# Optimization experiments

Measured on AMD Instinct MI355X. Metric: run time of the kernel, lower is better.

Reference implementation:

```python
import jax, jax.numpy as jnp
import numpy as np
import math

D_MODEL = 1024
N_HEAD = 16
Q_DIM = K_DIM = V_DIM = 1024
SCALE = math.sqrt(D_MODEL // N_HEAD)  # 8.0
B, LQ, LK = 2, 2048, 2048


def setup_inputs() -> dict:
    key = jax.random.key(0)
    ks = jax.random.split(key, 10)
    s = 1.0 / math.sqrt(Q_DIM)
    return {
        "q": jax.random.normal(ks[0], (B, LQ, Q_DIM), jnp.float32),
        "k": jax.random.normal(ks[1], (B, LK, K_DIM), jnp.float32),
        "v": jax.random.normal(ks[2], (B, LK, V_DIM), jnp.float32),
        "mask": jax.random.randint(ks[3], (B, LQ, LK), 0, 2, jnp.int32),
        "Wq": jax.random.uniform(ks[4], (D_MODEL, Q_DIM), jnp.float32, -s, s),
        "bq": jnp.zeros((D_MODEL,), jnp.float32),
        "Wk": jax.random.uniform(ks[5], (D_MODEL, K_DIM), jnp.float32, -s, s),
        "bk": jnp.zeros((D_MODEL,), jnp.float32),
        "Wv": jax.random.uniform(ks[6], (D_MODEL, V_DIM), jnp.float32, -s, s),
        "bv": jnp.zeros((D_MODEL,), jnp.float32),
    }


def reference(q, k, v, Wq, bq, Wk, bk, Wv, bv, mask):
    b, lq, _ = q.shape
    lk = k.shape[1]
    dh = D_MODEL // N_HEAD
    # linear projections (torch Linear: x @ W.T + b)
    qh = (q @ Wq.T + bq).reshape(b, lq, N_HEAD, dh).transpose(0, 2, 1, 3)  # bhqd
    kh = (k @ Wk.T + bk).reshape(b, lk, N_HEAD, dh).transpose(0, 2, 1, 3)  # bhkd
    vh = (v @ Wv.T + bv).reshape(b, lk, N_HEAD, dh).transpose(0, 2, 1, 3)  # bhkd
    attn = jnp.einsum("bhqd,bhkd->bhqk", qh, kh) / SCALE
    m = mask[:, None, :, :]  # b1qk
    attn = jnp.where(m == 0, -jnp.inf, attn)
    # rows whose mask is all-zero are reset to 0 pre-softmax (-> uniform weights)
    row_empty = (m.sum(-1, keepdims=True) == 0)
    attn = jnp.where(row_empty, 0.0, attn)
    attn = jax.nn.softmax(attn, axis=-1)  # dropout is identity in eval mode
    v_out = jnp.einsum("bhqk,bhkd->bhqd", attn, vh)
    v_out = v_out.transpose(0, 2, 1, 3).reshape(b, lq, D_MODEL)
    k_out = jnp.einsum("bhqk,bhkd->bhqd", attn, kh)
    k_out = k_out.transpose(0, 2, 1, 3).reshape(b, lq, D_MODEL)
    return (k_out, v_out)
```

## Files before the change

kernel.cpp:

```cpp
#include <hip/hip_runtime.h>
#include <hip/hip_bf16.h>
#include <stdint.h>

typedef __bf16 bf16x8 __attribute__((ext_vector_type(8)));
typedef __bf16 bf16x4 __attribute__((ext_vector_type(4)));
typedef float f32x4 __attribute__((ext_vector_type(4)));

#define B_ 2
#define LQ_ 2048
#define LK_ 2048
#define NH_ 16
#define DH_ 64
#define DM_ 1024

#define AS1 __attribute__((address_space(1)))
#define AS3 __attribute__((address_space(3)))

__device__ __forceinline__ void gload_lds16(const void* g, void* l) {
  __builtin_amdgcn_global_load_lds((const AS1 uint32_t*)g, (AS3 uint32_t*)l, 16, 0, 0);
}

__global__ __launch_bounds__(256) void pack_mask_kernel(
    const int* __restrict__ m, unsigned* __restrict__ out) {
  int gtid = blockIdx.x * 256 + threadIdx.x;
  unsigned long long bal = __ballot(m[gtid] != 0);
  if ((threadIdx.x & 31) == 0)
    out[gtid >> 5] = (unsigned)(bal >> ((threadIdx.x & 32) ? 32 : 0));
}

__global__ __launch_bounds__(256) void cvt_f32_bf16_kernel(
    const float* __restrict__ s, __bf16* __restrict__ d) {
  size_t t = (size_t)blockIdx.x * 256 + threadIdx.x;
  float4 f = ((const float4*)s)[t];
  bf16x4 o;
  o[0] = (__bf16)f.x; o[1] = (__bf16)f.y; o[2] = (__bf16)f.z; o[3] = (__bf16)f.w;
  ((bf16x4*)d)[t] = o;
}

__global__ __launch_bounds__(256) void proj_kernel(
    const __bf16* __restrict__ X0, const __bf16* __restrict__ X1,
    const __bf16* __restrict__ X2,
    const float* __restrict__ b0p, const float* __restrict__ b1p,
    const float* __restrict__ b2p,
    const __bf16* __restrict__ W0, const __bf16* __restrict__ W1,
    const __bf16* __restrict__ W2,
    __bf16* __restrict__ qh, __bf16* __restrict__ kh,
    __bf16* __restrict__ khT, __bf16* __restrict__ vhT, int zbase) {
  __shared__ __align__(16) __bf16 abuf[128 * 32];
  __shared__ __align__(16) __bf16 bbuf[128 * 32];
  __shared__ __align__(16) __bf16 c_lds[128][72];

  const int mode = zbase + blockIdx.z;
  const __bf16* X = mode == 0 ? X0 : (mode == 1 ? X1 : X2);
  const __bf16* W = mode == 0 ? W0 : (mode == 1 ? W1 : W2);
  const float* bias = mode == 0 ? b0p : (mode == 1 ? b1p : b2p);
  __bf16* ostd = mode == 0 ? qh : (mode == 1 ? kh : nullptr);
  __bf16* otr = mode == 0 ? nullptr : (mode == 1 ? khT : vhT);

  const int t = threadIdx.x;
  const int wave = t >> 6, lane = t & 63;
  const int lo16 = lane & 15, quad = lane >> 4;
  const int wm = wave >> 1, wn = wave & 1;
  const int m0 = blockIdx.x * 128, n0 = blockIdx.y * 128;
  const int srow = lane >> 2, scg = (lane & 3) ^ (srow & 3);

  f32x4 acc[4][4] = {};

  for (int k0 = 0; k0 < DM_; k0 += 32) {
    __syncthreads();
#pragma unroll
    for (int ii = 2 * wave; ii < 2 * wave + 2; ii++) {
      int row = ii * 16 + srow;
      gload_lds16(X + (size_t)(m0 + row) * DM_ + k0 + scg * 8, abuf + ii * 512);
      gload_lds16(W + (size_t)(n0 + row) * DM_ + k0 + scg * 8, bbuf + ii * 512);
    }
    __syncthreads();
    bf16x8 af[4], bfr[4];
#pragma unroll
    for (int g = 0; g < 4; g++) {
      int ar = wm * 64 + g * 16 + lo16;
      af[g] = *(const bf16x8*)(abuf + ar * 32 + (quad ^ (ar & 3)) * 8);
      int br = wn * 64 + g * 16 + lo16;
      bfr[g] = *(const bf16x8*)(bbuf + br * 32 + (quad ^ (br & 3)) * 8);
    }
#pragma unroll
    for (int gm = 0; gm < 4; gm++)
#pragma unroll
      for (int gn = 0; gn < 4; gn++)
        acc[gm][gn] =
            __builtin_amdgcn_mfma_f32_16x16x32_bf16(af[gm], bfr[gn], acc[gm][gn], 0, 0, 0);
  }

  const int b = m0 >> 11, l0 = m0 & 2047;
  for (int nhf = 0; nhf < 2; nhf++) {
    __syncthreads();
    if (wn == nhf) {
#pragma unroll
      for (int gn = 0; gn < 4; gn++) {
        float bi = bias[n0 + nhf * 64 + gn * 16 + lo16];
#pragma unroll
        for (int gm = 0; gm < 4; gm++)
#pragma unroll
          for (int r = 0; r < 4; r++)
            c_lds[wm * 64 + gm * 16 + quad * 4 + r][gn * 16 + lo16] =
                (__bf16)(acc[gm][gn][r] + bi);
      }
    }
    __syncthreads();
    int h = (n0 >> 6) + nhf;
    int bh = b * NH_ + h;
    if (ostd) {
      int m = t >> 1, coff = (t & 1) * 32;
      __bf16* dst = ostd + ((size_t)bh * LQ_ + l0 + m) * DH_ + coff;
#pragma unroll
      for (int j = 0; j < 4; j++)
        *(bf16x8*)(dst + j * 8) = *(const bf16x8*)&c_lds[m][coff + j * 8];
    }
    if (otr) {
      int d = t >> 2, mc = (t & 3) * 32;
      __align__(16) __bf16 tmp[32];
#pragma unroll
      for (int j = 0; j < 32; j++) tmp[j] = c_lds[mc + j][d];
      __bf16* dst = otr + ((size_t)bh * DH_ + d) * LK_ + l0 + mc;
#pragma unroll
      for (int j = 0; j < 4; j++)
        *(bf16x8*)(dst + j * 8) = *(const bf16x8*)&tmp[j * 8];
    }
  }
}

__global__ __launch_bounds__(256) void attn_kernel(
    const __bf16* __restrict__ qh, const __bf16* __restrict__ kh,
    const __bf16* __restrict__ khT, const __bf16* __restrict__ vhT,
    const unsigned* __restrict__ maskp,
    float* __restrict__ out_k, float* __restrict__ out_v) {
  __shared__ __align__(16) __bf16 kbuf[64 * 64];
  __shared__ __align__(16) __bf16 ktbuf[64 * 64];
  __shared__ __align__(16) __bf16 vtbuf[64 * 64];
  __shared__ __align__(16) __bf16 p_lds[4][16][72];

  const int t = threadIdx.x;
  const int wave = t >> 6, lane = t & 63;
  const int lo16 = lane & 15, quad = lane >> 4;
  const int bh = blockIdx.x;
  const int b = bh >> 4, h = bh & 15;
  const int q0 = blockIdx.y * 64 + wave * 16;
  const int srow = lane >> 3;
  const int scg = (lane & 7) ^ srow;
  const int rsw = lo16 & 7;

  const __bf16* qrow = qh + ((size_t)bh * LQ_ + q0 + lo16) * DH_ + quad * 8;
  bf16x8 a_q0 = *(const bf16x8*)(qrow);
  bf16x8 a_q1 = *(const bf16x8*)(qrow + 32);

  f32x4 acc_v[4] = {};
  f32x4 acc_k[4] = {};
  float lsum[4] = {0.f, 0.f, 0.f, 0.f};

  const __bf16* khb = kh + (size_t)bh * LK_ * DH_;
  const __bf16* khTb = khT + (size_t)bh * DH_ * LK_;
  const __bf16* vhTb = vhT + (size_t)bh * DH_ * LK_;
  const unsigned* mb = maskp + ((size_t)b * LQ_ + q0 + quad * 4) * (LK_ / 32);

  for (int kt = 0; kt < LK_; kt += 64) {
    __syncthreads();
#pragma unroll
    for (int ii = 2 * wave; ii < 2 * wave + 2; ii++) {
      int row = ii * 8 + srow;
      gload_lds16(khb + (size_t)(kt + row) * DH_ + scg * 8, kbuf + ii * 512);
      gload_lds16(khTb + (size_t)row * LK_ + kt + scg * 8, ktbuf + ii * 512);
      gload_lds16(vhTb + (size_t)row * LK_ + kt + scg * 8, vtbuf + ii * 512);
    }
    __syncthreads();
    f32x4 s[4];
#pragma unroll
    for (int g = 0; g < 4; g++) {
      int row = g * 16 + lo16;
      bf16x8 kb0 = *(const bf16x8*)(kbuf + row * 64 + (quad ^ rsw) * 8);
      bf16x8 kb1 = *(const bf16x8*)(kbuf + row * 64 + ((quad + 4) ^ rsw) * 8);
      f32x4 z = {};
      z = __builtin_amdgcn_mfma_f32_16x16x32_bf16(a_q0, kb0, z, 0, 0, 0);
      z = __builtin_amdgcn_mfma_f32_16x16x32_bf16(a_q1, kb1, z, 0, 0, 0);
      s[g] = z;
    }
    unsigned mw0[4], mw1[4];
#pragma unroll
    for (int r = 0; r < 4; r++) {
      mw0[r] = mb[(size_t)r * (LK_ / 32) + (kt >> 5)];
      mw1[r] = mb[(size_t)r * (LK_ / 32) + (kt >> 5) + 1];
    }
#pragma unroll
    for (int g = 0; g < 4; g++) {
      int bitpos = (g * 16 + lo16) & 31;
#pragma unroll
      for (int r = 0; r < 4; r++) {
        unsigned w = (g >= 2) ? mw1[r] : mw0[r];
        float arg = ((w >> bitpos) & 1) ? s[g][r] * 0.125f : -28.0f;
        float p = __expf(arg);
        s[g][r] = p;
        lsum[r] += p;
      }
    }
#pragma unroll
    for (int g = 0; g < 4; g++) {
#pragma unroll
      for (int r = 0; r < 4; r++)
        p_lds[wave][quad * 4 + r][g * 16 + lo16] = (__bf16)s[g][r];
    }
    bf16x8 a_p0 = *(const bf16x8*)&p_lds[wave][lo16][quad * 8];
    bf16x8 a_p1 = *(const bf16x8*)&p_lds[wave][lo16][32 + quad * 8];
#pragma unroll
    for (int g = 0; g < 4; g++) {
      int row = g * 16 + lo16;
      bf16x8 bv0 = *(const bf16x8*)(vtbuf + row * 64 + (quad ^ rsw) * 8);
      bf16x8 bv1 = *(const bf16x8*)(vtbuf + row * 64 + ((quad + 4) ^ rsw) * 8);
      acc_v[g] = __builtin_amdgcn_mfma_f32_16x16x32_bf16(a_p0, bv0, acc_v[g], 0, 0, 0);
      acc_v[g] = __builtin_amdgcn_mfma_f32_16x16x32_bf16(a_p1, bv1, acc_v[g], 0, 0, 0);
      bf16x8 bk0 = *(const bf16x8*)(ktbuf + row * 64 + (quad ^ rsw) * 8);
      bf16x8 bk1 = *(const bf16x8*)(ktbuf + row * 64 + ((quad + 4) ^ rsw) * 8);
      acc_k[g] = __builtin_amdgcn_mfma_f32_16x16x32_bf16(a_p0, bk0, acc_k[g], 0, 0, 0);
      acc_k[g] = __builtin_amdgcn_mfma_f32_16x16x32_bf16(a_p1, bk1, acc_k[g], 0, 0, 0);
    }
  }

#pragma unroll
  for (int off = 1; off < 16; off <<= 1) {
#pragma unroll
    for (int r = 0; r < 4; r++) lsum[r] += __shfl_xor(lsum[r], off, 64);
  }
  float inv_l[4];
#pragma unroll
  for (int r = 0; r < 4; r++) inv_l[r] = 1.0f / lsum[r];

  size_t obase = ((size_t)b * LQ_ + q0 + quad * 4) * DM_ + h * DH_;
#pragma unroll
  for (int g = 0; g < 4; g++) {
#pragma unroll
    for (int r = 0; r < 4; r++) {
      size_t idx = obase + (size_t)r * DM_ + g * 16 + lo16;
      out_k[idx] = acc_k[g][r] * inv_l[r];
      out_v[idx] = acc_v[g][r] * inv_l[r];
    }
  }
}

extern "C" void kernel_launch(void* const* d_in, const int* in_sizes, int n_in,
                              void* d_out, int out_size, void* d_ws, size_t ws_size,
                              hipStream_t stream) {
  const float* q = (const float*)d_in[0];
  const float* k = (const float*)d_in[1];
  const float* v = (const float*)d_in[2];
  const int* mask = (const int*)d_in[3];
  const float* Wq = (const float*)d_in[4];
  const float* bq = (const float*)d_in[5];
  const float* Wk = (const float*)d_in[6];
  const float* bk = (const float*)d_in[7];
  const float* Wv = (const float*)d_in[8];
  const float* bv = (const float*)d_in[9];
  float* out = (float*)d_out;

  const size_t HTOT = (size_t)B_ * NH_ * LQ_ * DH_;
  const size_t XTOT = (size_t)B_ * LQ_ * DM_;
  __bf16* qh = (__bf16*)d_ws;
  __bf16* kh = qh + HTOT;
  __bf16* khT = kh + HTOT;
  __bf16* vhT = khT + HTOT;
  unsigned* maskp = (unsigned*)(vhT + HTOT);
  __bf16* Wqb = (__bf16*)(maskp + (size_t)B_ * LQ_ * LK_ / 32);
  __bf16* Wkb = Wqb + (size_t)DM_ * DM_;
  __bf16* Wvb = Wkb + (size_t)DM_ * DM_;
  __bf16* X0 = Wvb + (size_t)DM_ * DM_;
  size_t need3 = (size_t)((char*)(X0 + 3 * XTOT) - (char*)d_ws);
  bool big = ws_size >= need3;

  pack_mask_kernel<<<(B_ * LQ_ * LK_) / 256, 256, 0, stream>>>(mask, maskp);
  cvt_f32_bf16_kernel<<<DM_ * DM_ / 1024, 256, 0, stream>>>(Wq, Wqb);
  cvt_f32_bf16_kernel<<<DM_ * DM_ / 1024, 256, 0, stream>>>(Wk, Wkb);
  cvt_f32_bf16_kernel<<<DM_ * DM_ / 1024, 256, 0, stream>>>(Wv, Wvb);

  if (big) {
    __bf16* X1 = X0 + XTOT;
    __bf16* X2 = X1 + XTOT;
    cvt_f32_bf16_kernel<<<XTOT / 1024, 256, 0, stream>>>(q, X0);
    cvt_f32_bf16_kernel<<<XTOT / 1024, 256, 0, stream>>>(k, X1);
    cvt_f32_bf16_kernel<<<XTOT / 1024, 256, 0, stream>>>(v, X2);
    proj_kernel<<<dim3(32, 8, 3), 256, 0, stream>>>(
        X0, X1, X2, bq, bk, bv, Wqb, Wkb, Wvb, qh, kh, khT, vhT, 0);
  } else {
    const float* xs[3] = {q, k, v};
    for (int i = 0; i < 3; i++) {
      cvt_f32_bf16_kernel<<<XTOT / 1024, 256, 0, stream>>>(xs[i], X0);
      proj_kernel<<<dim3(32, 8, 1), 256, 0, stream>>>(
          X0, X0, X0, bq, bk, bv, Wqb, Wkb, Wvb, qh, kh, khT, vhT, i);
    }
  }

  attn_kernel<<<dim3(32, 32), 256, 0, stream>>>(qh, kh, khT, vhT, maskp,
                                                out, out + (size_t)B_ * LQ_ * DM_);
}
```

Before: 316.4 us.

## Tile transposed K/V per 64-key block, drop LDS staging in attention

The projection kernel now writes K^T and V^T as contiguous 64x64 tiles per key block. This lets the attention kernel read MFMA operands straight from global memory with no LDS staging and no __syncthreads. The six conversion launches are merged into one kernel. The bf16 staging buffers move into the output buffer, which removes the small-workspace fallback path. The trade is that every wave now issues uncoalesced-ish direct global loads per tile, relying on L2/L1 reuse across the four waves instead of shared memory.

```diff
diff --git a/kernel.cpp b/kernel.cpp
--- a/kernel.cpp
+++ b/kernel.cpp
@@ -12,6 +12,7 @@
 #define NH_ 16
 #define DH_ 64
 #define DM_ 1024
+#define NKT_ (LK_ / 64)
 
 #define AS1 __attribute__((address_space(1)))
 #define AS3 __attribute__((address_space(3)))
@@ -28,8 +29,18 @@
     out[gtid >> 5] = (unsigned)(bal >> ((threadIdx.x & 32) ? 32 : 0));
 }
 
-__global__ __launch_bounds__(256) void cvt_f32_bf16_kernel(
-    const float* __restrict__ s, __bf16* __restrict__ d) {
+__global__ __launch_bounds__(256) void cvt6_kernel(
+    const float* __restrict__ q, const float* __restrict__ k,
+    const float* __restrict__ v, const float* __restrict__ wq,
+    const float* __restrict__ wk, const float* __restrict__ wv,
+    __bf16* __restrict__ X0, __bf16* __restrict__ X1, __bf16* __restrict__ X2,
+    __bf16* __restrict__ W0, __bf16* __restrict__ W1, __bf16* __restrict__ W2) {
+  int seg = blockIdx.y;
+  if (seg >= 3 && blockIdx.x >= DM_ * DM_ / 1024) return;
+  const float* s = seg == 0 ? q : seg == 1 ? k : seg == 2 ? v
+                  : seg == 3 ? wq : seg == 4 ? wk : wv;
+  __bf16* d = seg == 0 ? X0 : seg == 1 ? X1 : seg == 2 ? X2
+             : seg == 3 ? W0 : seg == 4 ? W1 : W2;
   size_t t = (size_t)blockIdx.x * 256 + threadIdx.x;
   float4 f = ((const float4*)s)[t];
   bf16x4 o;
@@ -45,12 +56,12 @@
     const __bf16* __restrict__ W0, const __bf16* __restrict__ W1,
     const __bf16* __restrict__ W2,
     __bf16* __restrict__ qh, __bf16* __restrict__ kh,
-    __bf16* __restrict__ khT, __bf16* __restrict__ vhT, int zbase) {
+    __bf16* __restrict__ khT, __bf16* __restrict__ vhT) {
   __shared__ __align__(16) __bf16 abuf[128 * 32];
   __shared__ __align__(16) __bf16 bbuf[128 * 32];
-  __shared__ __align__(16) __bf16 c_lds[128][72];
-
-  const int mode = zbase + blockIdx.z;
+  __shared__ __align__(16) __bf16 cbuf[128 * 72];
+
+  const int mode = blockIdx.z;
   const __bf16* X = mode == 0 ? X0 : (mode == 1 ? X1 : X2);
   const __bf16* W = mode == 0 ? W0 : (mode == 1 ? W1 : W2);
   const float* bias = mode == 0 ? b0p : (mode == 1 ? b1p : b2p);
@@ -93,38 +104,51 @@
 
   const int b = m0 >> 11, l0 = m0 & 2047;
   for (int nhf = 0; nhf < 2; nhf++) {
-    __syncthreads();
-    if (wn == nhf) {
-#pragma unroll
-      for (int gn = 0; gn < 4; gn++) {
-        float bi = bias[n0 + nhf * 64 + gn * 16 + lo16];
-#pragma unroll
-        for (int gm = 0; gm < 4; gm++)
-#pragma unroll
-          for (int r = 0; r < 4; r++)
-            c_lds[wm * 64 + gm * 16 + quad * 4 + r][gn * 16 + lo16] =
-                (__bf16)(acc[gm][gn][r] + bi);
-      }
-    }
-    __syncthreads();
     int h = (n0 >> 6) + nhf;
     int bh = b * NH_ + h;
     if (ostd) {
+      __syncthreads();
+      if (wn == nhf) {
+#pragma unroll
+        for (int gn = 0; gn < 4; gn++) {
+          float bi = bias[n0 + nhf * 64 + gn * 16 + lo16];
+#pragma unroll
+          for (int gm = 0; gm < 4; gm++)
+#pragma unroll
+            for (int r = 0; r < 4; r++)
+              cbuf[(wm * 64 + gm * 16 + quad * 4 + r) * 72 + gn * 16 + lo16] =
+                  (__bf16)(acc[gm][gn][r] + bi);
+        }
+      }
+      __syncthreads();
       int m = t >> 1, coff = (t & 1) * 32;
       __bf16* dst = ostd + ((size_t)bh * LQ_ + l0 + m) * DH_ + coff;
 #pragma unroll
       for (int j = 0; j < 4; j++)
-        *(bf16x8*)(dst + j * 8) = *(const bf16x8*)&c_lds[m][coff + j * 8];
+        *(bf16x8*)(dst + j * 8) = *(const bf16x8*)&cbuf[m * 72 + coff + j * 8];
     }
     if (otr) {
+      __syncthreads();
+      if (wn == nhf) {
+#pragma unroll
+        for (int gn = 0; gn < 4; gn++) {
+          float bi = bias[n0 + nhf * 64 + gn * 16 + lo16];
+#pragma unroll
+          for (int gm = 0; gm < 4; gm++) {
+            bf16x4 pk;
+#pragma unroll
+            for (int r = 0; r < 4; r++) pk[r] = (__bf16)(acc[gm][gn][r] + bi);
+            *(bf16x4*)&cbuf[(gn * 16 + lo16) * 136 + wm * 64 + gm * 16 + quad * 4] = pk;
+          }
+        }
+      }
+      __syncthreads();
       int d = t >> 2, mc = (t & 3) * 32;
-      __align__(16) __bf16 tmp[32];
-#pragma unroll
-      for (int j = 0; j < 32; j++) tmp[j] = c_lds[mc + j][d];
-      __bf16* dst = otr + ((size_t)bh * DH_ + d) * LK_ + l0 + mc;
+      int kti = (l0 + mc) >> 6, kl = (l0 + mc) & 63;
+      __bf16* dst = otr + ((size_t)(bh * NKT_ + kti) * 64 + d) * 64 + kl;
 #pragma unroll
       for (int j = 0; j < 4; j++)
-        *(bf16x8*)(dst + j * 8) = *(const bf16x8*)&tmp[j * 8];
+        *(bf16x8*)(dst + j * 8) = *(const bf16x8*)&cbuf[d * 136 + mc + j * 8];
     }
   }
 }
@@ -134,9 +158,6 @@
     const __bf16* __restrict__ khT, const __bf16* __restrict__ vhT,
     const unsigned* __restrict__ maskp,
     float* __restrict__ out_k, float* __restrict__ out_v) {
-  __shared__ __align__(16) __bf16 kbuf[64 * 64];
-  __shared__ __align__(16) __bf16 ktbuf[64 * 64];
-  __shared__ __align__(16) __bf16 vtbuf[64 * 64];
   __shared__ __align__(16) __bf16 p_lds[4][16][72];
 
   const int t = threadIdx.x;
@@ -145,9 +166,6 @@
   const int bh = blockIdx.x;
   const int b = bh >> 4, h = bh & 15;
   const int q0 = blockIdx.y * 64 + wave * 16;
-  const int srow = lane >> 3;
-  const int scg = (lane & 7) ^ srow;
-  const int rsw = lo16 & 7;
 
   const __bf16* qrow = qh + ((size_t)bh * LQ_ + q0 + lo16) * DH_ + quad * 8;
   bf16x8 a_q0 = *(const bf16x8*)(qrow);
@@ -158,26 +176,19 @@
   float lsum[4] = {0.f, 0.f, 0.f, 0.f};
 
   const __bf16* khb = kh + (size_t)bh * LK_ * DH_;
-  const __bf16* khTb = khT + (size_t)bh * DH_ * LK_;
-  const __bf16* vhTb = vhT + (size_t)bh * DH_ * LK_;
+  const __bf16* ktb = khT + (size_t)bh * LK_ * DH_;
+  const __bf16* vtb = vhT + (size_t)bh * LK_ * DH_;
   const unsigned* mb = maskp + ((size_t)b * LQ_ + q0 + quad * 4) * (LK_ / 32);
-
-  for (int kt = 0; kt < LK_; kt += 64) {
-    __syncthreads();
-#pragma unroll
-    for (int ii = 2 * wave; ii < 2 * wave + 2; ii++) {
-      int row = ii * 8 + srow;
-      gload_lds16(khb + (size_t)(kt + row) * DH_ + scg * 8, kbuf + ii * 512);
-      gload_lds16(khTb + (size_t)row * LK_ + kt + scg * 8, ktbuf + ii * 512);
-      gload_lds16(vhTb + (size_t)row * LK_ + kt + scg * 8, vtbuf + ii * 512);
-    }
-    __syncthreads();
+  const int voff = lo16 * 64 + quad * 8;
+
+  for (int kti = 0; kti < NKT_; kti++) {
+    const int tb = kti * 4096;
     f32x4 s[4];
 #pragma unroll
     for (int g = 0; g < 4; g++) {
-      int row = g * 16 + lo16;
-      bf16x8 kb0 = *(const bf16x8*)(kbuf + row * 64 + (quad ^ rsw) * 8);
-      bf16x8 kb1 = *(const bf16x8*)(kbuf + row * 64 + ((quad + 4) ^ rsw) * 8);
+      const __bf16* p = khb + tb + g * 1024 + voff;
+      bf16x8 kb0 = *(const bf16x8*)(p);
+      bf16x8 kb1 = *(const bf16x8*)(p + 32);
       f32x4 z = {};
       z = __builtin_amdgcn_mfma_f32_16x16x32_bf16(a_q0, kb0, z, 0, 0, 0);
       z = __builtin_amdgcn_mfma_f32_16x16x32_bf16(a_q1, kb1, z, 0, 0, 0);
@@ -186,8 +197,8 @@
     unsigned mw0[4], mw1[4];
 #pragma unroll
     for (int r = 0; r < 4; r++) {
-      mw0[r] = mb[(size_t)r * (LK_ / 32) + (kt >> 5)];
-      mw1[r] = mb[(size_t)r * (LK_ / 32) + (kt >> 5) + 1];
+      mw0[r] = mb[r * (LK_ / 32) + kti * 2];
+      mw1[r] = mb[r * (LK_ / 32) + kti * 2 + 1];
     }
 #pragma unroll
     for (int g = 0; g < 4; g++) {
@@ -211,13 +222,14 @@
     bf16x8 a_p1 = *(const bf16x8*)&p_lds[wave][lo16][32 + quad * 8];
 #pragma unroll
     for (int g = 0; g < 4; g++) {
-      int row = g * 16 + lo16;
-      bf16x8 bv0 = *(const bf16x8*)(vtbuf + row * 64 + (quad ^ rsw) * 8);
-      bf16x8 bv1 = *(const bf16x8*)(vtbuf + row * 64 + ((quad + 4) ^ rsw) * 8);
+      const __bf16* pv = vtb + tb + g * 1024 + voff;
+      bf16x8 bv0 = *(const bf16x8*)(pv);
+      bf16x8 bv1 = *(const bf16x8*)(pv + 32);
       acc_v[g] = __builtin_amdgcn_mfma_f32_16x16x32_bf16(a_p0, bv0, acc_v[g], 0, 0, 0);
       acc_v[g] = __builtin_amdgcn_mfma_f32_16x16x32_bf16(a_p1, bv1, acc_v[g], 0, 0, 0);
-      bf16x8 bk0 = *(const bf16x8*)(ktbuf + row * 64 + (quad ^ rsw) * 8);
-      bf16x8 bk1 = *(const bf16x8*)(ktbuf + row * 64 + ((quad + 4) ^ rsw) * 8);
+      const __bf16* pk = ktb + tb + g * 1024 + voff;
+      bf16x8 bk0 = *(const bf16x8*)(pk);
+      bf16x8 bk1 = *(const bf16x8*)(pk + 32);
       acc_k[g] = __builtin_amdgcn_mfma_f32_16x16x32_bf16(a_p0, bk0, acc_k[g], 0, 0, 0);
       acc_k[g] = __builtin_amdgcn_mfma_f32_16x16x32_bf16(a_p1, bk1, acc_k[g], 0, 0, 0);
     }
@@ -266,35 +278,19 @@
   __bf16* khT = kh + HTOT;
   __bf16* vhT = khT + HTOT;
   unsigned* maskp = (unsigned*)(vhT + HTOT);
-  __bf16* Wqb = (__bf16*)(maskp + (size_t)B_ * LQ_ * LK_ / 32);
-  __bf16* Wkb = Wqb + (size_t)DM_ * DM_;
-  __bf16* Wvb = Wkb + (size_t)DM_ * DM_;
-  __bf16* X0 = Wvb + (size_t)DM_ * DM_;
-  size_t need3 = (size_t)((char*)(X0 + 3 * XTOT) - (char*)d_ws);
-  bool big = ws_size >= need3;
+
+  __bf16* X0 = (__bf16*)d_out;
+  __bf16* X1 = X0 + XTOT;
+  __bf16* X2 = X1 + XTOT;
+  __bf16* W0 = X2 + XTOT;
+  __bf16* W1 = W0 + (size_t)DM_ * DM_;
+  __bf16* W2 = W1 + (size_t)DM_ * DM_;
 
   pack_mask_kernel<<<(B_ * LQ_ * LK_) / 256, 256, 0, stream>>>(mask, maskp);
-  cvt_f32_bf16_kernel<<<DM_ * DM_ / 1024, 256, 0, stream>>>(Wq, Wqb);
-  cvt_f32_bf16_kernel<<<DM_ * DM_ / 1024, 256, 0, stream>>>(Wk, Wkb);
-  cvt_f32_bf16_kernel<<<DM_ * DM_ / 1024, 256, 0, stream>>>(Wv, Wvb);
-
-  if (big) {
-    __bf16* X1 = X0 + XTOT;
-    __bf16* X2 = X1 + XTOT;
-    cvt_f32_bf16_kernel<<<XTOT / 1024, 256, 0, stream>>>(q, X0);
-    cvt_f32_bf16_kernel<<<XTOT / 1024, 256, 0, stream>>>(k, X1);
-    cvt_f32_bf16_kernel<<<XTOT / 1024, 256, 0, stream>>>(v, X2);
-    proj_kernel<<<dim3(32, 8, 3), 256, 0, stream>>>(
-        X0, X1, X2, bq, bk, bv, Wqb, Wkb, Wvb, qh, kh, khT, vhT, 0);
-  } else {
-    const float* xs[3] = {q, k, v};
-    for (int i = 0; i < 3; i++) {
-      cvt_f32_bf16_kernel<<<XTOT / 1024, 256, 0, stream>>>(xs[i], X0);
-      proj_kernel<<<dim3(32, 8, 1), 256, 0, stream>>>(
-          X0, X0, X0, bq, bk, bv, Wqb, Wkb, Wvb, qh, kh, khT, vhT, i);
-    }
-  }
-
+  cvt6_kernel<<<dim3(XTOT / 1024, 6), 256, 0, stream>>>(
+      q, k, v, Wq, Wk, Wv, X0, X1, X2, W0, W1, W2);
+  proj_kernel<<<dim3(32, 8, 3), 256, 0, stream>>>(
+      X0, X1, X2, bq, bk, bv, W0, W1, W2, qh, kh, khT, vhT);
   attn_kernel<<<dim3(32, 32), 256, 0, stream>>>(qh, kh, khT, vhT, maskp,
                                                 out, out + (size_t)B_ * LQ_ * DM_);
 }
```

New measurement: 552.9 us. 74.8% more time.
